# Kernel tuning notes

Hardware: AMD Instinct MI355X
Metric: run time of the kernel (lower is better)

Reference implementation:

```python
import jax, jax.numpy as jnp
import numpy as np

N = 50000      # nodes
E = 1600000    # edges
H = 128        # hidden_dim
P = 28         # pocket_dim
G = 256        # graphs in the batch
EPS = 1e-5     # BatchNorm eps


def setup_inputs() -> dict:
    key = jax.random.key(0)
    ks = jax.random.split(key, 24)
    s = 0.05
    inp = {
        "x": jax.random.normal(ks[0], (N, 7), jnp.float32),
        "edge_index": jax.random.randint(ks[1], (2, E), 0, N, jnp.int64),
        "batch": jnp.sort(jax.random.randint(ks[2], (N,), 0, G, jnp.int64)),
        "pocket_features": jax.random.normal(ks[3], (P,), jnp.float32),
        # GCN conv weights (first layer 7->128, layers 2..3 stacked 128->128)
        "conv0_W": jax.random.normal(ks[4], (7, H), jnp.float32) * s,
        "conv0_b": jnp.zeros((H,), jnp.float32),
        "convs_W": jax.random.normal(ks[5], (2, H, H), jnp.float32) * s,
        "convs_b": jnp.zeros((2, H), jnp.float32),
        # BatchNorm (eval mode) params per layer, stacked [3, H]
        "bn_gamma": jnp.ones((3, H), jnp.float32),
        "bn_beta": jnp.zeros((3, H), jnp.float32),
        "bn_mean": jax.random.normal(ks[6], (3, H), jnp.float32) * 0.1,
        "bn_var": jax.random.uniform(ks[7], (3, H), jnp.float32, 0.5, 1.5),
        # pocket MLP 28->64->64
        "pmlp_W1": jax.random.normal(ks[8], (P, 64), jnp.float32) * s,
        "pmlp_b1": jnp.zeros((64,), jnp.float32),
        "pmlp_W2": jax.random.normal(ks[9], (64, 64), jnp.float32) * s,
        "pmlp_b2": jnp.zeros((64,), jnp.float32),
        # Bilinear: torch weight shape [out=64, in1=H, in2=64]
        "bil_W": jax.random.normal(ks[10], (64, H, 64), jnp.float32) * s,
        "bil_b": jnp.zeros((64,), jnp.float32),
        # classifier 64->32->1
        "cls_W1": jax.random.normal(ks[11], (64, 32), jnp.float32) * s,
        "cls_b1": jnp.zeros((32,), jnp.float32),
        "cls_W2": jax.random.normal(ks[12], (32, 1), jnp.float32) * s,
        "cls_b2": jnp.zeros((1,), jnp.float32),
    }
    return inp


def _gcn(x, W, b, src, dst, dinv):
    """PyG GCNConv: sym-normalized aggregation with added self loops."""
    h = x @ W                                  # [N, H']
    norm = dinv[src] * dinv[dst]               # [E]
    agg = jax.ops.segment_sum(norm[:, None] * h[src], dst, num_segments=N)
    agg = agg + (dinv * dinv)[:, None] * h     # self-loop contribution
    return agg + b


def reference(x, edge_index, batch, pocket_features,
              conv0_W, conv0_b, convs_W, convs_b,
              bn_gamma, bn_beta, bn_mean, bn_var,
              pmlp_W1, pmlp_b1, pmlp_W2, pmlp_b2,
              bil_W, bil_b, cls_W1, cls_b1, cls_W2, cls_b2):
    src, dst = edge_index[0], edge_index[1]
    # degree over targets, with +1 for the self loop
    deg = jax.ops.segment_sum(jnp.ones((E,), x.dtype), dst, num_segments=N) + 1.0
    dinv = jax.lax.rsqrt(deg)

    h = x
    for i in range(3):
        W = conv0_W if i == 0 else convs_W[i - 1]
        b = conv0_b if i == 0 else convs_b[i - 1]
        h = _gcn(h, W, b, src, dst, dinv)
        # BatchNorm1d in eval mode; dropout = identity in eval
        h = bn_gamma[i] * (h - bn_mean[i]) * jax.lax.rsqrt(bn_var[i] + EPS) + bn_beta[i]
        h = jax.nn.relu(h)

    # global_mean_pool over graph ids
    sums = jax.ops.segment_sum(h, batch, num_segments=G)              # [G, H]
    cnt = jax.ops.segment_sum(jnp.ones((N,), h.dtype), batch, num_segments=G)
    ligand = sums / jnp.maximum(cnt, 1.0)[:, None]                    # [G, H]

    pk = jax.nn.relu(pocket_features @ pmlp_W1 + pmlp_b1) @ pmlp_W2 + pmlp_b2  # [64]
    pk = jnp.broadcast_to(pk, (G, 64))

    inter = jnp.einsum('bi,oij,bj->bo', ligand, bil_W, pk) + bil_b    # [G, 64]
    z = jax.nn.relu(inter @ cls_W1 + cls_b1) @ cls_W2 + cls_b2        # [G, 1]
    return z[:, 0]
```

## Files before the change

kernel.cpp:

```cpp
#include <hip/hip_runtime.h>

#define EPSBN 1e-5f
#define BCAP 12288
#define CSRL_CAP 13312
#define OVCAP 262144
#define INS_CAP 24
#define INS_STRIDE 25

#if defined(__has_builtin)
#if __has_builtin(__builtin_amdgcn_cvt_pk_f32_fp8) && __has_builtin(__builtin_amdgcn_cvt_pk_fp8_f32)
#define HAS_CVT_FP8 1
#endif
#endif

typedef float v2f_t __attribute__((ext_vector_type(2)));
typedef __attribute__((ext_vector_type(8))) short bf16x8;
typedef __attribute__((ext_vector_type(4))) float f32x4;

__device__ inline unsigned short f2bf(float f) {
    unsigned int u = __float_as_uint(f);
    u += 0x7fffu + ((u >> 16) & 1u);
    return (unsigned short)(u >> 16);
}

__device__ inline float fp8_dec_byte(int b) {
    int s = (b >> 7) & 1, e = (b >> 3) & 15, m = b & 7;
    float v = (e == 0) ? ldexpf((float)m, -9) : ldexpf((float)(8 + m), e - 10);
    return s ? -v : v;
}
__device__ inline unsigned int fp8_enc(float x) {
    unsigned int u = __float_as_uint(x);
    unsigned int s = u >> 31;
    u &= 0x7fffffffu;
    float a = __uint_as_float(u);
    unsigned int code;
    if (a >= 0.015625f) {
        if (a > 448.0f) code = 0x7E;
        else {
            int exp = (int)(u >> 23) - 127;
            unsigned int mant = u & 0x7fffffu;
            unsigned int keep = mant >> 20;
            unsigned int rest = mant & 0xfffffu;
            code = ((unsigned int)(exp + 7) << 3) | keep;
            unsigned int rnd = (rest > 0x80000u) || (rest == 0x80000u && (code & 1));
            code += rnd;
            if (code > 0x7E) code = 0x7E;
        }
    } else {
        code = (unsigned int)(a * 512.0f + 0.5f);
    }
    return (s << 7) | code;
}

__device__ __forceinline__ void fp8x8_dec(uint2 w, float* v) {
#ifdef HAS_CVT_FP8
    v2f_t l0 = __builtin_amdgcn_cvt_pk_f32_fp8((int)w.x, false);
    v2f_t h0 = __builtin_amdgcn_cvt_pk_f32_fp8((int)w.x, true);
    v2f_t l1 = __builtin_amdgcn_cvt_pk_f32_fp8((int)w.y, false);
    v2f_t h1 = __builtin_amdgcn_cvt_pk_f32_fp8((int)w.y, true);
    v[0] = l0[0]; v[1] = l0[1]; v[2] = h0[0]; v[3] = h0[1];
    v[4] = l1[0]; v[5] = l1[1]; v[6] = h1[0]; v[7] = h1[1];
#else
    v[0] = fp8_dec_byte(w.x & 255);        v[1] = fp8_dec_byte((w.x >> 8) & 255);
    v[2] = fp8_dec_byte((w.x >> 16) & 255); v[3] = fp8_dec_byte(w.x >> 24);
    v[4] = fp8_dec_byte(w.y & 255);        v[5] = fp8_dec_byte((w.y >> 8) & 255);
    v[6] = fp8_dec_byte((w.y >> 16) & 255); v[7] = fp8_dec_byte(w.y >> 24);
#endif
}

__global__ void setup_kernel(int* __restrict__ tails, int ntail,
                             const int* __restrict__ batch, int* __restrict__ gstart,
                             int n, int g,
                             const float* __restrict__ conv0_b, const float* __restrict__ convs_b,
                             const float* __restrict__ gamma, const float* __restrict__ beta,
                             const float* __restrict__ mean, const float* __restrict__ var,
                             float* __restrict__ sc, float* __restrict__ sh,
                             const float* __restrict__ convs_W, unsigned short* __restrict__ Wp,
                             const float* __restrict__ pf, const float* __restrict__ W1,
                             const float* __restrict__ b1, const float* __restrict__ W2,
                             const float* __restrict__ b2, const float* __restrict__ bilW,
                             float* __restrict__ M) {
    int t = threadIdx.x;
    int i = blockIdx.x * 256 + t;
    if (i < ntail * 32) tails[i] = 0;
    if (i < 384) {
        int l = i >> 7, f = i & 127;
        float bias = (l == 0) ? conv0_b[f] : convs_b[(l - 1) * 128 + f];
        float s = gamma[i] * rsqrtf(var[i] + EPSBN);
        sc[i] = s;
        sh[i] = fmaf(s, bias - mean[i], beta[i]);
    }
    if (i < 32768) {
        int l = i >> 14;
        int fidx = i & 16383;
        int j  = fidx & 7;
        int ln = (fidx >> 3) & 63;
        int nt = (fidx >> 9) & 7;
        int kk = fidx >> 12;
        int k = kk * 32 + (ln >> 4) * 8 + j;
        int c = nt * 16 + (ln & 15);
        Wp[i] = f2bf(convs_W[l * 16384 + k * 128 + c]);
    }
    if (i < n) {
        int b = batch[i];
        int bp = (i == 0) ? -1 : batch[i - 1];
        for (int q = bp + 1; q <= b; ++q) gstart[q] = i;
        if (i == n - 1) {
            for (int q = b + 1; q <= g; ++q) gstart[q] = n;
        }
    }
    if (blockIdx.x < 32) {
        __shared__ float h1s[64];
        __shared__ float spk[64];
        if (t < 64) {
            float acc = b1[t];
            #pragma unroll
            for (int k = 0; k < 28; ++k) acc = fmaf(pf[k], W1[k * 64 + t], acc);
            h1s[t] = fmaxf(acc, 0.f);
        }
        __syncthreads();
        if (t < 64) {
            float acc2 = b2[t];
            for (int k = 0; k < 64; ++k) acc2 = fmaf(h1s[k], W2[k * 64 + t], acc2);
            spk[t] = acc2;
        }
        __syncthreads();
        if (i < 64 * 128) {
            const float* wr = bilW + (size_t)i * 64;
            float acc = 0.f;
            #pragma unroll 8
            for (int j = 0; j < 64; ++j) acc = fmaf(wr[j], spk[j], acc);
            M[i] = acc;
        }
    }
}

__launch_bounds__(256)
__global__ void bucket_kernel(const int* __restrict__ src, const int* __restrict__ dst,
                              unsigned int* __restrict__ buckets, int* __restrict__ tails,
                              unsigned int* __restrict__ ovf, int e, int nwq) {
    __shared__ unsigned int buf[256 * INS_STRIDE];
    __shared__ int cnt[256];
    __shared__ int basee[256];
    int t = threadIdx.x;
    cnt[t] = 0;
    __syncthreads();
    int c0 = blockIdx.x * 2048;
    int c1 = min(c0 + 2048, e);
    for (int i = c0 + t; i < c1; i += 256) {
        int d = dst[i];
        int bb = d >> 8;
        unsigned int val = (unsigned int)src[i] | ((unsigned int)d << 16);
        int pos = atomicAdd(&cnt[bb], 1);
        if (pos < INS_CAP) buf[bb * INS_STRIDE + pos] = val;
        else {
            int op = atomicAdd(&tails[nwq * 32], 1);
            if (op < OVCAP) ovf[op] = val;
        }
    }
    __syncthreads();
    int lane = t & 63, wv = t >> 6;
    int bb0 = wv * 64;
    {
        int b = bb0 + lane;
        int c = (b < nwq) ? min(cnt[b], INS_CAP) : 0;
        basee[b] = c ? atomicAdd(&tails[b * 32], c) : 0;
    }
    for (int k = 0; k < 64; ++k) {
        int b = bb0 + k;
        if (b >= nwq) break;
        int c = min(cnt[b], INS_CAP);
        if (c == 0) continue;
        int g = basee[b];
        if (lane < c) {
            unsigned int v = buf[b * INS_STRIDE + lane];
            int gp = g + lane;
            if (gp < BCAP) buckets[(size_t)b * BCAP + gp] = v;
            else {
                int op = atomicAdd(&tails[nwq * 32], 1);
                if (op < OVCAP) ovf[op] = v;
            }
        }
    }
}

__launch_bounds__(256)
__global__ void build_csr(const unsigned int* __restrict__ buckets,
                          const int* __restrict__ tails, const unsigned int* __restrict__ ovf,
                          unsigned short* __restrict__ csr, int* __restrict__ deg,
                          int* __restrict__ offs, float* __restrict__ dinv,
                          int n, int nwq) {
    __shared__ unsigned short csrL[CSRL_CAP];
    __shared__ int degL[256], curL[256], offsL[256], cntW[256];
    __shared__ int wsum4[4];
    __shared__ int wstart;
    int b = blockIdx.x, t = threadIdx.x;
    int lo = b << 8;
    int hi = min(lo + 256, n);
    int nw = hi - lo;
    int ovn = min(tails[nwq * 32], OVCAP);
    cntW[t] = (t < nwq) ? min(tails[t * 32], BCAP) : 0;
    degL[t] = 0;
    __syncthreads();
    for (int i = t; i < ovn; i += 256)
        atomicAdd(&cntW[(ovf[i] >> 16) >> 8], 1);
    __syncthreads();
    if (t == 0) {
        int s = 0;
        for (int w = 0; w < b; ++w) s += cntW[w];
        wstart = s;
    }
    int myvalid = min(tails[b * 32], BCAP);
    const unsigned int* myb = buckets + (size_t)b * BCAP;
    for (int i = t; i < myvalid; i += 256)
        atomicAdd(&degL[(myb[i] >> 16) & 255], 1);
    for (int i = t; i < ovn; i += 256) {
        unsigned int v = ovf[i];
        int d = v >> 16;
        if (d >= lo && d < hi) atomicAdd(&degL[d & 255], 1);
    }
    __syncthreads();
    {
        int lane = t & 63, wv = t >> 6;
        int v = degL[t];
        int sc0 = v;
        #pragma unroll
        for (int o = 1; o < 64; o <<= 1) {
            int u = __shfl_up(sc0, o);
            if (lane >= o) sc0 += u;
        }
        if (lane == 63) wsum4[wv] = sc0;
        __syncthreads();
        int wb = 0;
        for (int q = 0; q < wv; ++q) wb += wsum4[q];
        offsL[t] = wb + sc0 - v;
        curL[t] = offsL[t];
    }
    __syncthreads();
    for (int i = t; i < myvalid; i += 256) {
        unsigned int v = myb[i];
        int pos = atomicAdd(&curL[(v >> 16) & 255], 1);
        if (pos < CSRL_CAP) csrL[pos] = (unsigned short)(v & 0xffffu);
    }
    for (int i = t; i < ovn; i += 256) {
        unsigned int v = ovf[i];
        int d = v >> 16;
        if (d >= lo && d < hi) {
            int pos = atomicAdd(&curL[d & 255], 1);
            if (pos < CSRL_CAP) csrL[pos] = (unsigned short)(v & 0xffffu);
        }
    }
    __syncthreads();
    int base = wstart;
    int total = min(cntW[b], CSRL_CAP);
    for (int i = t; i < total; i += 256)
        csr[base + i] = csrL[i];
    if (t < nw) {
        int dgi = degL[t];
        deg[lo + t] = dgi;
        offs[lo + t] = base + offsL[t];
        dinv[lo + t] = rsqrtf((float)dgi + 1.0f);
    }
}

__device__ __forceinline__ void dense_fp8_out(const unsigned short* hL,
                                              const unsigned short* __restrict__ Wp,
                                              unsigned char* __restrict__ out8,
                                              int b0n, int n, int lane, int wv) {
    f32x4 acc0 = {0.f, 0.f, 0.f, 0.f};
    f32x4 acc1 = {0.f, 0.f, 0.f, 0.f};
    int r = lane & 15, g = lane >> 4;
    int nt0 = wv * 2, nt1 = nt0 + 1;
    #pragma unroll
    for (int kk = 0; kk < 4; ++kk) {
        bf16x8 a  = *(const bf16x8*)(hL + r * 136 + kk * 32 + g * 8);
        bf16x8 b0 = *(const bf16x8*)(Wp + ((kk * 8 + nt0) * 64 + lane) * 8);
        bf16x8 b1 = *(const bf16x8*)(Wp + ((kk * 8 + nt1) * 64 + lane) * 8);
        acc0 = __builtin_amdgcn_mfma_f32_16x16x32_bf16(a, b0, acc0, 0, 0, 0);
        acc1 = __builtin_amdgcn_mfma_f32_16x16x32_bf16(a, b1, acc1, 0, 0, 0);
    }
    #pragma unroll
    for (int j = 0; j < 4; ++j) {
        int node = b0n + g * 4 + j;
        if (node < n) {
            unsigned char q0, q1;
#ifdef HAS_CVT_FP8
            q0 = (unsigned char)(__builtin_amdgcn_cvt_pk_fp8_f32(acc0[j], acc0[j], 0, false) & 0xff);
            q1 = (unsigned char)(__builtin_amdgcn_cvt_pk_fp8_f32(acc1[j], acc1[j], 0, false) & 0xff);
#else
            q0 = (unsigned char)fp8_enc(acc0[j]);
            q1 = (unsigned char)fp8_enc(acc1[j]);
#endif
            out8[(size_t)node * 128 + nt0 * 16 + r] = q0;
            out8[(size_t)node * 128 + nt1 * 16 + r] = q1;
        }
    }
}

__launch_bounds__(256)
__global__ void layer0f_kernel(const float* __restrict__ x, const unsigned short* __restrict__ csr,
                               const int* __restrict__ offs, const int* __restrict__ degi,
                               const float* __restrict__ dinv, const float* __restrict__ W,
                               const float* __restrict__ sc, const float* __restrict__ sh,
                               const unsigned short* __restrict__ Wp,
                               unsigned char* __restrict__ out8, int n) {
    __shared__ float sW[7 * 128];
    __shared__ float ssc[128], ssh[128];
    __shared__ unsigned short hL[16 * 136];
    int t = threadIdx.x;
    for (int i = t; i < 7 * 128; i += 256) sW[i] = W[i];
    if (t < 128) { ssc[t] = sc[t]; ssh[t] = sh[t]; }
    __syncthreads();
    int lane = t & 63, wv = t >> 6;
    int b0n = blockIdx.x * 16;
    int e = lane >> 3, f = lane & 7;
    for (int nd = 0; nd < 4; ++nd) {
        int node = b0n + wv * 4 + nd;
        if (node < n) {
            int off = offs[node], cnt = degi[node];
            float di = dinv[node];
            float acc = 0.f, accB = 0.f;
            for (int b0 = 0; b0 < cnt; b0 += 64) {
                int j = b0 + lane;
                int s = 0; float dv = 0.f;
                if (j < cnt) { s = csr[off + j]; dv = dinv[s]; }
                int m = cnt - b0; if (m > 64) m = 64;
                int m16 = (m + 15) & ~15;
                for (int i2 = 0; i2 < m16; i2 += 16) {
                    int ss1 = __shfl(s, i2 + e);
                    int ss2 = __shfl(s, i2 + 8 + e);
                    float d1 = __shfl(dv, i2 + e);
                    float d2 = __shfl(dv, i2 + 8 + e);
                    float v1 = 0.f, v2 = 0.f;
                    if (f < 7) {
                        v1 = d1 * x[(size_t)ss1 * 7 + f];
                        v2 = d2 * x[(size_t)ss2 * 7 + f];
                    }
                    acc += v1; accB += v2;
                }
            }
            acc += accB;
            acc += __shfl_xor(acc, 8);
            acc += __shfl_xor(acc, 16);
            acc += __shfl_xor(acc, 32);
            float self = (f < 7) ? x[(size_t)node * 7 + f] : 0.f;
            float xa = di * (acc + di * self);
            float xk[7];
            #pragma unroll
            for (int k = 0; k < 7; ++k) xk[k] = __shfl(xa, k);
            int fo = lane * 2;
            float o0 = 0.f, o1 = 0.f;
            #pragma unroll
            for (int k = 0; k < 7; ++k) {
                o0 = fmaf(xk[k], sW[k * 128 + fo], o0);
                o1 = fmaf(xk[k], sW[k * 128 + fo + 1], o1);
            }
            o0 = fmaxf(fmaf(ssc[fo],     o0, ssh[fo]),     0.f);
            o1 = fmaxf(fmaf(ssc[fo + 1], o1, ssh[fo + 1]), 0.f);
            unsigned int p = (unsigned int)f2bf(o0) | ((unsigned int)f2bf(o1) << 16);
            *(unsigned int*)(&hL[(wv * 4 + nd) * 136 + fo]) = p;
        }
    }
    __syncthreads();
    dense_fp8_out(hL, Wp, out8, b0n, n, lane, wv);
}

template<int DENSE>
__launch_bounds__(256)
__global__ void aggf_kernel(const unsigned int* __restrict__ hw, const unsigned short* __restrict__ csr,
                            const int* __restrict__ offs, const int* __restrict__ degi,
                            const float* __restrict__ dinv,
                            const float* __restrict__ sc, const float* __restrict__ shv,
                            const unsigned short* __restrict__ Wp,
                            unsigned char* __restrict__ out8,
                            float* __restrict__ outF, int n) {
    __shared__ unsigned short hL[16 * 136];
    int t = threadIdx.x, lane = t & 63, wv = t >> 6;
    int fl = lane & 15, grp = lane >> 4;
    int b0n = blockIdx.x * 16;
    for (int nd = 0; nd < 4; ++nd) {
        int node = b0n + wv * 4 + nd;
        if (node < n) {
            float di = dinv[node];
            int off = offs[node], cnt = degi[node];
            float a[8];
            #pragma unroll
            for (int i = 0; i < 8; ++i) a[i] = 0.f;
            for (int c0 = 0; c0 < cnt; c0 += 64) {
                int j = c0 + lane;
                int s = 0; float dv = 0.f;
                if (j < cnt) { s = csr[off + j]; dv = dinv[s]; }
                int m = cnt - c0; if (m > 64) m = 64;
                int m16 = (m + 15) & ~15;
                for (int e = 0; e < m16; e += 16) {
                    #pragma unroll
                    for (int u = 0; u < 4; ++u) {
                        int jj = e + u * 4 + grp;
                        int ss = __shfl(s, jj);
                        float nn = __shfl(dv, jj);
                        uint2 w = *(const uint2*)(hw + (size_t)ss * 32 + fl * 2);
                        float v[8];
                        fp8x8_dec(w, v);
                        #pragma unroll
                        for (int i = 0; i < 8; ++i) a[i] = fmaf(nn, v[i], a[i]);
                    }
                }
            }
            #pragma unroll
            for (int i = 0; i < 8; ++i) {
                a[i] += __shfl_xor(a[i], 16);
                a[i] += __shfl_xor(a[i], 32);
            }
            if (grp == 0) {
                uint2 ws = *(const uint2*)(hw + (size_t)node * 32 + fl * 2);
                float sv[8];
                fp8x8_dec(ws, sv);
                int f0 = fl * 8;
                float vo[8];
                #pragma unroll
                for (int i = 0; i < 8; ++i) {
                    float vv = (a[i] + di * sv[i]) * di;
                    vo[i] = fmaxf(fmaf(sc[f0 + i], vv, shv[f0 + i]), 0.f);
                }
                if (DENSE) {
                    uint4 P;
                    P.x = (unsigned int)f2bf(vo[0]) | ((unsigned int)f2bf(vo[1]) << 16);
                    P.y = (unsigned int)f2bf(vo[2]) | ((unsigned int)f2bf(vo[3]) << 16);
                    P.z = (unsigned int)f2bf(vo[4]) | ((unsigned int)f2bf(vo[5]) << 16);
                    P.w = (unsigned int)f2bf(vo[6]) | ((unsigned int)f2bf(vo[7]) << 16);
                    *(uint4*)(&hL[(wv * 4 + nd) * 136 + f0]) = P;
                } else {
                    float4 o0 = make_float4(vo[0], vo[1], vo[2], vo[3]);
                    float4 o1 = make_float4(vo[4], vo[5], vo[6], vo[7]);
                    *(float4*)(outF + (size_t)node * 128 + f0)     = o0;
                    *(float4*)(outF + (size_t)node * 128 + f0 + 4) = o1;
                }
            }
        }
    }
    if (DENSE) {
        __syncthreads();
        dense_fp8_out(hL, Wp, out8, b0n, n, lane, wv);
    }
}

__launch_bounds__(128)
__global__ void final_kernel(const float* __restrict__ h, const int* __restrict__ gstart,
                             const float* __restrict__ M, const float* __restrict__ bil_b,
                             const float* __restrict__ cW1, const float* __restrict__ cb1,
                             const float* __restrict__ cW2, const float* __restrict__ cb2,
                             float* __restrict__ out) {
    __shared__ float lig[128];
    __shared__ float inter[64];
    __shared__ float hc[32];
    int g = blockIdx.x, t = threadIdx.x;
    int s = gstart[g], e = gstart[g + 1];
    float a0 = 0.f, a1 = 0.f, a2 = 0.f, a3 = 0.f;
    int i = s;
    for (; i + 4 <= e; i += 4) {
        a0 += h[(size_t)(i + 0) * 128 + t];
        a1 += h[(size_t)(i + 1) * 128 + t];
        a2 += h[(size_t)(i + 2) * 128 + t];
        a3 += h[(size_t)(i + 3) * 128 + t];
    }
    for (; i < e; ++i) a0 += h[(size_t)i * 128 + t];
    float c = (float)(e - s); if (c < 1.f) c = 1.f;
    lig[t] = ((a0 + a1) + (a2 + a3)) / c;
    __syncthreads();
    if (t < 64) {
        float acc = bil_b[t];
        const float* mr = M + (size_t)t * 128;
        #pragma unroll 8
        for (int k = 0; k < 128; ++k) acc = fmaf(lig[k], mr[k], acc);
        inter[t] = acc;
    }
    __syncthreads();
    if (t < 32) {
        float acc = cb1[t];
        #pragma unroll 8
        for (int o = 0; o < 64; ++o) acc = fmaf(inter[o], cW1[o * 32 + t], acc);
        hc[t] = fmaxf(acc, 0.f);
    }
    __syncthreads();
    if (t == 0) {
        float acc = cb2[0];
        #pragma unroll
        for (int j = 0; j < 32; ++j) acc = fmaf(hc[j], cW2[j], acc);
        out[g] = acc;
    }
}

extern "C" void kernel_launch(void* const* d_in, const int* in_sizes, int n_in,
                              void* d_out, int out_size, void* d_ws, size_t ws_size,
                              hipStream_t stream) {
    const float* x        = (const float*)d_in[0];
    const int*   edge     = (const int*)d_in[1];
    const int*   batch    = (const int*)d_in[2];
    const float* pocket   = (const float*)d_in[3];
    const float* conv0_W  = (const float*)d_in[4];
    const float* conv0_b  = (const float*)d_in[5];
    const float* convs_W  = (const float*)d_in[6];
    const float* convs_b  = (const float*)d_in[7];
    const float* bn_gamma = (const float*)d_in[8];
    const float* bn_beta  = (const float*)d_in[9];
    const float* bn_mean  = (const float*)d_in[10];
    const float* bn_var   = (const float*)d_in[11];
    const float* pmlp_W1  = (const float*)d_in[12];
    const float* pmlp_b1  = (const float*)d_in[13];
    const float* pmlp_W2  = (const float*)d_in[14];
    const float* pmlp_b2  = (const float*)d_in[15];
    const float* bil_W    = (const float*)d_in[16];
    const float* bil_b    = (const float*)d_in[17];
    const float* cls_W1   = (const float*)d_in[18];
    const float* cls_b1   = (const float*)d_in[19];
    const float* cls_W2   = (const float*)d_in[20];
    const float* cls_b2   = (const float*)d_in[21];

    const int N = in_sizes[0] / 7;
    const int E = in_sizes[1] / 2;
    const int G = out_size;
    const int* srcA = edge;
    const int* dstA = edge + E;
    const int NB  = (N + 255) / 256;
    const int NWQ = (N + 255) >> 8;
    const int NBL = (N + 15) / 16;

    char* p = (char*)d_ws;
    auto alloc = [&](size_t bytes) -> void* {
        void* r = (void*)p;
        p += (bytes + 255) & ~(size_t)255;
        return r;
    };
    int*   tails    = (int*)alloc((size_t)(NWQ + 1) * 32 * 4);
    unsigned int* buckets = (unsigned int*)alloc((size_t)NWQ * BCAP * 4);
    unsigned int* ovf     = (unsigned int*)alloc((size_t)OVCAP * 4);
    int*   deg      = (int*)alloc((size_t)N * 4);
    int*   offs     = (int*)alloc((size_t)N * 4);
    float* dinv     = (float*)alloc((size_t)N * 4);
    unsigned short* csr = (unsigned short*)alloc((size_t)E * 2);
    unsigned char* bufH8a = (unsigned char*)alloc((size_t)N * 128);
    unsigned char* bufH8b = (unsigned char*)alloc((size_t)N * 128);
    float* bufF     = (float*)alloc((size_t)N * 128 * 4);
    int*   gstart   = (int*)alloc((size_t)(G + 1) * 4);
    float* M        = (float*)alloc(64 * 128 * 4);
    float* sc       = (float*)alloc(384 * 4);
    float* shv      = (float*)alloc(384 * 4);
    unsigned short* Wp = (unsigned short*)alloc((size_t)2 * 16384 * 2);

    setup_kernel<<<NB, 256, 0, stream>>>(tails, NWQ + 1, batch, gstart, N, G,
                                         conv0_b, convs_b, bn_gamma, bn_beta, bn_mean, bn_var,
                                         sc, shv, convs_W, Wp,
                                         pocket, pmlp_W1, pmlp_b1, pmlp_W2, pmlp_b2, bil_W, M);
    bucket_kernel<<<(E + 2047) / 2048, 256, 0, stream>>>(srcA, dstA, buckets, tails, ovf,
                                                         E, NWQ);
    build_csr<<<NWQ, 256, 0, stream>>>(buckets, tails, ovf, csr, deg, offs, dinv, N, NWQ);

    layer0f_kernel<<<NBL, 256, 0, stream>>>(x, csr, offs, deg, dinv, conv0_W,
                                            sc, shv, Wp, bufH8a, N);
    aggf_kernel<1><<<NBL, 256, 0, stream>>>((const unsigned int*)bufH8a, csr, offs, deg, dinv,
                                            sc + 128, shv + 128, Wp + 16384, bufH8b, nullptr, N);
    aggf_kernel<0><<<NBL, 256, 0, stream>>>((const unsigned int*)bufH8b, csr, offs, deg, dinv,
                                            sc + 256, shv + 256, nullptr, nullptr, bufF, N);

    final_kernel<<<G, 128, 0, stream>>>(bufF, gstart, M, bil_b, cls_W1, cls_b1, cls_W2, cls_b2,
                                        (float*)d_out);
}
```

Baseline: 284.2 us.

## Pack source dinv into padded CSR entries and compute degrees during bucketing

Degrees are now counted with global atomics in the bucketing pass, and a separate kernel computes dinv and per-window padded sizes. The CSR becomes 32-bit entries that pack the source id with a bf16 copy of its dinv, and each node's list is padded to a multiple of 16 with zero entries. This removes the dependent dinv[src] gather and the shuffle broadcasts from the aggregation loops and lets each lane load edges directly with unrolled independent gathers. In exchange it adds global atomics, an extra launch, larger CSR traffic, and bf16 rounding of the normalisation; the final pooling loop is also unrolled to 8 accumulators.

```diff
diff --git a/kernel.cpp b/kernel.cpp
--- a/kernel.cpp
+++ b/kernel.cpp
@@ -2,7 +2,6 @@
 
 #define EPSBN 1e-5f
 #define BCAP 12288
-#define CSRL_CAP 13312
 #define OVCAP 262144
 #define INS_CAP 24
 #define INS_STRIDE 25
@@ -70,6 +69,7 @@
 
 __global__ void setup_kernel(int* __restrict__ tails, int ntail,
                              const int* __restrict__ batch, int* __restrict__ gstart,
+                             int* __restrict__ deg,
                              int n, int g,
                              const float* __restrict__ conv0_b, const float* __restrict__ convs_b,
                              const float* __restrict__ gamma, const float* __restrict__ beta,
@@ -102,6 +102,7 @@
         Wp[i] = f2bf(convs_W[l * 16384 + k * 128 + c]);
     }
     if (i < n) {
+        deg[i] = 0;
         int b = batch[i];
         int bp = (i == 0) ? -1 : batch[i - 1];
         for (int q = bp + 1; q <= b; ++q) gstart[q] = i;
@@ -138,7 +139,8 @@
 __launch_bounds__(256)
 __global__ void bucket_kernel(const int* __restrict__ src, const int* __restrict__ dst,
                               unsigned int* __restrict__ buckets, int* __restrict__ tails,
-                              unsigned int* __restrict__ ovf, int e, int nwq) {
+                              unsigned int* __restrict__ ovf, int* __restrict__ deg,
+                              int e, int nwq) {
     __shared__ unsigned int buf[256 * INS_STRIDE];
     __shared__ int cnt[256];
     __shared__ int basee[256];
@@ -150,6 +152,7 @@
     for (int i = c0 + t; i < c1; i += 256) {
         int d = dst[i];
         int bb = d >> 8;
+        atomicAdd(&deg[d], 1);
         unsigned int val = (unsigned int)src[i] | ((unsigned int)d << 16);
         int pos = atomicAdd(&cnt[bb], 1);
         if (pos < INS_CAP) buf[bb * INS_STRIDE + pos] = val;
@@ -185,82 +188,86 @@
 }
 
 __launch_bounds__(256)
-__global__ void build_csr(const unsigned int* __restrict__ buckets,
-                          const int* __restrict__ tails, const unsigned int* __restrict__ ovf,
-                          unsigned short* __restrict__ csr, int* __restrict__ deg,
-                          int* __restrict__ offs, float* __restrict__ dinv,
-                          int n, int nwq) {
-    __shared__ unsigned short csrL[CSRL_CAP];
-    __shared__ int degL[256], curL[256], offsL[256], cntW[256];
+__global__ void dinv_kernel(const int* __restrict__ deg, float* __restrict__ dinv,
+                            int* __restrict__ winPad, int n) {
+    __shared__ int ws[4];
+    int b = blockIdx.x, t = threadIdx.x;
+    int i = b * 256 + t;
+    int d = (i < n) ? deg[i] : 0;
+    if (i < n) dinv[i] = rsqrtf((float)d + 1.0f);
+    int pad = (i < n) ? ((d + 15) & ~15) : 0;
+    int lane = t & 63, wv = t >> 6;
+    int s = pad;
+    #pragma unroll
+    for (int o = 1; o < 64; o <<= 1) s += __shfl_xor(s, o);
+    if (lane == 0) ws[wv] = s;
+    __syncthreads();
+    if (t == 0) winPad[b] = ws[0] + ws[1] + ws[2] + ws[3];
+}
+
+__launch_bounds__(256)
+__global__ void build_csr2(const unsigned int* __restrict__ buckets,
+                           const int* __restrict__ tails, const unsigned int* __restrict__ ovf,
+                           const int* __restrict__ deg, const float* __restrict__ dinv,
+                           const int* __restrict__ winPad,
+                           unsigned int* __restrict__ csr2, int* __restrict__ offs,
+                           int n, int nwq) {
+    __shared__ int curL[256];
     __shared__ int wsum4[4];
     __shared__ int wstart;
     int b = blockIdx.x, t = threadIdx.x;
     int lo = b << 8;
     int hi = min(lo + 256, n);
     int nw = hi - lo;
-    int ovn = min(tails[nwq * 32], OVCAP);
-    cntW[t] = (t < nwq) ? min(tails[t * 32], BCAP) : 0;
-    degL[t] = 0;
-    __syncthreads();
-    for (int i = t; i < ovn; i += 256)
-        atomicAdd(&cntW[(ovf[i] >> 16) >> 8], 1);
-    __syncthreads();
     if (t == 0) {
         int s = 0;
-        for (int w = 0; w < b; ++w) s += cntW[w];
+        for (int w = 0; w < b; ++w) s += winPad[w];
         wstart = s;
     }
+    int dpad = (t < nw) ? ((deg[lo + t] + 15) & ~15) : 0;
+    int lane = t & 63, wv = t >> 6;
+    int sc0 = dpad;
+    #pragma unroll
+    for (int o = 1; o < 64; o <<= 1) {
+        int u = __shfl_up(sc0, o);
+        if (lane >= o) sc0 += u;
+    }
+    if (lane == 63) wsum4[wv] = sc0;
+    __syncthreads();
+    int wb = 0;
+    for (int q = 0; q < wv; ++q) wb += wsum4[q];
+    int myoff = wb + sc0 - dpad;
+    curL[t] = myoff;
+    int total = wsum4[0] + wsum4[1] + wsum4[2] + wsum4[3];
+    int base = wstart;
+    for (int i = t; i < total; i += 256) csr2[base + i] = 0u;
+    __syncthreads();
     int myvalid = min(tails[b * 32], BCAP);
     const unsigned int* myb = buckets + (size_t)b * BCAP;
-    for (int i = t; i < myvalid; i += 256)
-        atomicAdd(&degL[(myb[i] >> 16) & 255], 1);
-    for (int i = t; i < ovn; i += 256) {
-        unsigned int v = ovf[i];
-        int d = v >> 16;
-        if (d >= lo && d < hi) atomicAdd(&degL[d & 255], 1);
-    }
-    __syncthreads();
-    {
-        int lane = t & 63, wv = t >> 6;
-        int v = degL[t];
-        int sc0 = v;
-        #pragma unroll
-        for (int o = 1; o < 64; o <<= 1) {
-            int u = __shfl_up(sc0, o);
-            if (lane >= o) sc0 += u;
-        }
-        if (lane == 63) wsum4[wv] = sc0;
-        __syncthreads();
-        int wb = 0;
-        for (int q = 0; q < wv; ++q) wb += wsum4[q];
-        offsL[t] = wb + sc0 - v;
-        curL[t] = offsL[t];
-    }
-    __syncthreads();
     for (int i = t; i < myvalid; i += 256) {
         unsigned int v = myb[i];
-        int pos = atomicAdd(&curL[(v >> 16) & 255], 1);
-        if (pos < CSRL_CAP) csrL[pos] = (unsigned short)(v & 0xffffu);
-    }
+        int dl = (v >> 16) & 255;
+        int s = v & 0xffff;
+        int pos = atomicAdd(&curL[dl], 1);
+        if (pos < total) {
+            unsigned int enc = (unsigned int)f2bf(dinv[s]);
+            csr2[base + pos] = (unsigned int)s | (enc << 16);
+        }
+    }
+    int ovn = min(tails[nwq * 32], OVCAP);
     for (int i = t; i < ovn; i += 256) {
         unsigned int v = ovf[i];
         int d = v >> 16;
         if (d >= lo && d < hi) {
+            int s = v & 0xffff;
             int pos = atomicAdd(&curL[d & 255], 1);
-            if (pos < CSRL_CAP) csrL[pos] = (unsigned short)(v & 0xffffu);
-        }
-    }
-    __syncthreads();
-    int base = wstart;
-    int total = min(cntW[b], CSRL_CAP);
-    for (int i = t; i < total; i += 256)
-        csr[base + i] = csrL[i];
-    if (t < nw) {
-        int dgi = degL[t];
-        deg[lo + t] = dgi;
-        offs[lo + t] = base + offsL[t];
-        dinv[lo + t] = rsqrtf((float)dgi + 1.0f);
-    }
+            if (pos < total) {
+                unsigned int enc = (unsigned int)f2bf(dinv[s]);
+                csr2[base + pos] = (unsigned int)s | (enc << 16);
+            }
+        }
+    }
+    if (t < nw) offs[lo + t] = base + myoff;
 }
 
 __device__ __forceinline__ void dense_fp8_out(const unsigned short* hL,
@@ -298,7 +305,7 @@
 }
 
 __launch_bounds__(256)
-__global__ void layer0f_kernel(const float* __restrict__ x, const unsigned short* __restrict__ csr,
+__global__ void layer0f_kernel(const float* __restrict__ x, const unsigned int* __restrict__ csr2,
                                const int* __restrict__ offs, const int* __restrict__ degi,
                                const float* __restrict__ dinv, const float* __restrict__ W,
                                const float* __restrict__ sc, const float* __restrict__ sh,
@@ -316,34 +323,30 @@
     int e = lane >> 3, f = lane & 7;
     for (int nd = 0; nd < 4; ++nd) {
         int node = b0n + wv * 4 + nd;
-        if (node < n) {
-            int off = offs[node], cnt = degi[node];
-            float di = dinv[node];
-            float acc = 0.f, accB = 0.f;
-            for (int b0 = 0; b0 < cnt; b0 += 64) {
-                int j = b0 + lane;
-                int s = 0; float dv = 0.f;
-                if (j < cnt) { s = csr[off + j]; dv = dinv[s]; }
-                int m = cnt - b0; if (m > 64) m = 64;
-                int m16 = (m + 15) & ~15;
-                for (int i2 = 0; i2 < m16; i2 += 16) {
-                    int ss1 = __shfl(s, i2 + e);
-                    int ss2 = __shfl(s, i2 + 8 + e);
-                    float d1 = __shfl(dv, i2 + e);
-                    float d2 = __shfl(dv, i2 + 8 + e);
-                    float v1 = 0.f, v2 = 0.f;
-                    if (f < 7) {
-                        v1 = d1 * x[(size_t)ss1 * 7 + f];
-                        v2 = d2 * x[(size_t)ss2 * 7 + f];
-                    }
-                    acc += v1; accB += v2;
-                }
-            }
-            acc += accB;
+        bool ok = node < n;
+        int off  = ok ? offs[node] : 0;
+        int cntp = ok ? ((degi[node] + 15) & ~15) : 0;
+        float di = ok ? dinv[node] : 0.f;
+        float self = (ok && f < 7) ? x[(size_t)node * 7 + f] : 0.f;
+        float acc = 0.f;
+        for (int c0 = 0; c0 < cntp; c0 += 16) {
+            unsigned int e4[2];
+            #pragma unroll
+            for (int u = 0; u < 2; ++u) e4[u] = csr2[off + c0 + u * 8 + e];
+            float vA[2];
+            #pragma unroll
+            for (int u = 0; u < 2; ++u) {
+                int ss = e4[u] & 0xffff;
+                vA[u] = (f < 7) ? x[(size_t)ss * 7 + f] : 0.f;
+            }
+            #pragma unroll
+            for (int u = 0; u < 2; ++u)
+                acc = fmaf(__uint_as_float(e4[u] & 0xffff0000u), vA[u], acc);
+        }
+        if (ok) {
             acc += __shfl_xor(acc, 8);
             acc += __shfl_xor(acc, 16);
             acc += __shfl_xor(acc, 32);
-            float self = (f < 7) ? x[(size_t)node * 7 + f] : 0.f;
             float xa = di * (acc + di * self);
             float xk[7];
             #pragma unroll
@@ -367,7 +370,7 @@
 
 template<int DENSE>
 __launch_bounds__(256)
-__global__ void aggf_kernel(const unsigned int* __restrict__ hw, const unsigned short* __restrict__ csr,
+__global__ void aggf_kernel(const unsigned int* __restrict__ hw, const unsigned int* __restrict__ csr2,
                             const int* __restrict__ offs, const int* __restrict__ degi,
                             const float* __restrict__ dinv,
                             const float* __restrict__ sc, const float* __restrict__ shv,
@@ -380,61 +383,60 @@
     int b0n = blockIdx.x * 16;
     for (int nd = 0; nd < 4; ++nd) {
         int node = b0n + wv * 4 + nd;
-        if (node < n) {
-            float di = dinv[node];
-            int off = offs[node], cnt = degi[node];
-            float a[8];
-            #pragma unroll
-            for (int i = 0; i < 8; ++i) a[i] = 0.f;
-            for (int c0 = 0; c0 < cnt; c0 += 64) {
-                int j = c0 + lane;
-                int s = 0; float dv = 0.f;
-                if (j < cnt) { s = csr[off + j]; dv = dinv[s]; }
-                int m = cnt - c0; if (m > 64) m = 64;
-                int m16 = (m + 15) & ~15;
-                for (int e = 0; e < m16; e += 16) {
-                    #pragma unroll
-                    for (int u = 0; u < 4; ++u) {
-                        int jj = e + u * 4 + grp;
-                        int ss = __shfl(s, jj);
-                        float nn = __shfl(dv, jj);
-                        uint2 w = *(const uint2*)(hw + (size_t)ss * 32 + fl * 2);
-                        float v[8];
-                        fp8x8_dec(w, v);
-                        #pragma unroll
-                        for (int i = 0; i < 8; ++i) a[i] = fmaf(nn, v[i], a[i]);
-                    }
-                }
-            }
+        bool ok = node < n;
+        int off  = ok ? offs[node] : 0;
+        int cntp = ok ? ((degi[node] + 15) & ~15) : 0;
+        float di = ok ? dinv[node] : 0.f;
+        uint2 ws = ok ? *(const uint2*)(hw + (size_t)node * 32 + fl * 2) : make_uint2(0u, 0u);
+        float a[8];
+        #pragma unroll
+        for (int i = 0; i < 8; ++i) a[i] = 0.f;
+        for (int c0 = 0; c0 < cntp; c0 += 16) {
+            unsigned int e4[4];
+            #pragma unroll
+            for (int u = 0; u < 4; ++u) e4[u] = csr2[off + c0 + u * 4 + grp];
+            uint2 w[4];
+            #pragma unroll
+            for (int u = 0; u < 4; ++u) {
+                int ss = e4[u] & 0xffff;
+                w[u] = *(const uint2*)(hw + (size_t)ss * 32 + fl * 2);
+            }
+            #pragma unroll
+            for (int u = 0; u < 4; ++u) {
+                float nn = __uint_as_float(e4[u] & 0xffff0000u);
+                float v[8];
+                fp8x8_dec(w[u], v);
+                #pragma unroll
+                for (int i = 0; i < 8; ++i) a[i] = fmaf(nn, v[i], a[i]);
+            }
+        }
+        #pragma unroll
+        for (int i = 0; i < 8; ++i) {
+            a[i] += __shfl_xor(a[i], 16);
+            a[i] += __shfl_xor(a[i], 32);
+        }
+        if (grp == 0 && ok) {
+            float sv[8];
+            fp8x8_dec(ws, sv);
+            int f0 = fl * 8;
+            float vo[8];
             #pragma unroll
             for (int i = 0; i < 8; ++i) {
-                a[i] += __shfl_xor(a[i], 16);
-                a[i] += __shfl_xor(a[i], 32);
-            }
-            if (grp == 0) {
-                uint2 ws = *(const uint2*)(hw + (size_t)node * 32 + fl * 2);
-                float sv[8];
-                fp8x8_dec(ws, sv);
-                int f0 = fl * 8;
-                float vo[8];
-                #pragma unroll
-                for (int i = 0; i < 8; ++i) {
-                    float vv = (a[i] + di * sv[i]) * di;
-                    vo[i] = fmaxf(fmaf(sc[f0 + i], vv, shv[f0 + i]), 0.f);
-                }
-                if (DENSE) {
-                    uint4 P;
-                    P.x = (unsigned int)f2bf(vo[0]) | ((unsigned int)f2bf(vo[1]) << 16);
-                    P.y = (unsigned int)f2bf(vo[2]) | ((unsigned int)f2bf(vo[3]) << 16);
-                    P.z = (unsigned int)f2bf(vo[4]) | ((unsigned int)f2bf(vo[5]) << 16);
-                    P.w = (unsigned int)f2bf(vo[6]) | ((unsigned int)f2bf(vo[7]) << 16);
-                    *(uint4*)(&hL[(wv * 4 + nd) * 136 + f0]) = P;
-                } else {
-                    float4 o0 = make_float4(vo[0], vo[1], vo[2], vo[3]);
-                    float4 o1 = make_float4(vo[4], vo[5], vo[6], vo[7]);
-                    *(float4*)(outF + (size_t)node * 128 + f0)     = o0;
-                    *(float4*)(outF + (size_t)node * 128 + f0 + 4) = o1;
-                }
+                float vv = (a[i] + di * sv[i]) * di;
+                vo[i] = fmaxf(fmaf(sc[f0 + i], vv, shv[f0 + i]), 0.f);
+            }
+            if (DENSE) {
+                uint4 P;
+                P.x = (unsigned int)f2bf(vo[0]) | ((unsigned int)f2bf(vo[1]) << 16);
+                P.y = (unsigned int)f2bf(vo[2]) | ((unsigned int)f2bf(vo[3]) << 16);
+                P.z = (unsigned int)f2bf(vo[4]) | ((unsigned int)f2bf(vo[5]) << 16);
+                P.w = (unsigned int)f2bf(vo[6]) | ((unsigned int)f2bf(vo[7]) << 16);
+                *(uint4*)(&hL[(wv * 4 + nd) * 136 + f0]) = P;
+            } else {
+                float4 o0 = make_float4(vo[0], vo[1], vo[2], vo[3]);
+                float4 o1 = make_float4(vo[4], vo[5], vo[6], vo[7]);
+                *(float4*)(outF + (size_t)node * 128 + f0)     = o0;
+                *(float4*)(outF + (size_t)node * 128 + f0 + 4) = o1;
             }
         }
     }
@@ -455,17 +457,18 @@
     __shared__ float hc[32];
     int g = blockIdx.x, t = threadIdx.x;
     int s = gstart[g], e = gstart[g + 1];
-    float a0 = 0.f, a1 = 0.f, a2 = 0.f, a3 = 0.f;
+    float a[8];
+    #pragma unroll
+    for (int q = 0; q < 8; ++q) a[q] = 0.f;
     int i = s;
-    for (; i + 4 <= e; i += 4) {
-        a0 += h[(size_t)(i + 0) * 128 + t];
-        a1 += h[(size_t)(i + 1) * 128 + t];
-        a2 += h[(size_t)(i + 2) * 128 + t];
-        a3 += h[(size_t)(i + 3) * 128 + t];
-    }
-    for (; i < e; ++i) a0 += h[(size_t)i * 128 + t];
+    for (; i + 8 <= e; i += 8) {
+        #pragma unroll
+        for (int q = 0; q < 8; ++q)
+            a[q] += h[(size_t)(i + q) * 128 + t];
+    }
+    for (; i < e; ++i) a[0] += h[(size_t)i * 128 + t];
     float c = (float)(e - s); if (c < 1.f) c = 1.f;
-    lig[t] = ((a0 + a1) + (a2 + a3)) / c;
+    lig[t] = (((a[0] + a[1]) + (a[2] + a[3])) + ((a[4] + a[5]) + (a[6] + a[7]))) / c;
     __syncthreads();
     if (t < 64) {
         float acc = bil_b[t];
@@ -537,7 +540,8 @@
     int*   deg      = (int*)alloc((size_t)N * 4);
     int*   offs     = (int*)alloc((size_t)N * 4);
     float* dinv     = (float*)alloc((size_t)N * 4);
-    unsigned short* csr = (unsigned short*)alloc((size_t)E * 2);
+    int*   winPad   = (int*)alloc((size_t)NWQ * 4);
+    unsigned int* csr2 = (unsigned int*)alloc(((size_t)E + 15 * (size_t)N + 4096) * 4);
     unsigned char* bufH8a = (unsigned char*)alloc((size_t)N * 128);
     unsigned char* bufH8b = (unsigned char*)alloc((size_t)N * 128);
     float* bufF     = (float*)alloc((size_t)N * 128 * 4);
@@ -547,19 +551,21 @@
     float* shv      = (float*)alloc(384 * 4);
     unsigned short* Wp = (unsigned short*)alloc((size_t)2 * 16384 * 2);
 
-    setup_kernel<<<NB, 256, 0, stream>>>(tails, NWQ + 1, batch, gstart, N, G,
+    setup_kernel<<<NB, 256, 0, stream>>>(tails, NWQ + 1, batch, gstart, deg, N, G,
                                          conv0_b, convs_b, bn_gamma, bn_beta, bn_mean, bn_var,
                                          sc, shv, convs_W, Wp,
                                          pocket, pmlp_W1, pmlp_b1, pmlp_W2, pmlp_b2, bil_W, M);
-    bucket_kernel<<<(E + 2047) / 2048, 256, 0, stream>>>(srcA, dstA, buckets, tails, ovf,
+    bucket_kernel<<<(E + 2047) / 2048, 256, 0, stream>>>(srcA, dstA, buckets, tails, ovf, deg,
                                                          E, NWQ);
-    build_csr<<<NWQ, 256, 0, stream>>>(buckets, tails, ovf, csr, deg, offs, dinv, N, NWQ);
-
-    layer0f_kernel<<<NBL, 256, 0, stream>>>(x, csr, offs, deg, dinv, conv0_W,
+    dinv_kernel<<<NWQ, 256, 0, stream>>>(deg, dinv, winPad, N);
+    build_csr2<<<NWQ, 256, 0, stream>>>(buckets, tails, ovf, deg, dinv, winPad,
+                                        csr2, offs, N, NWQ);
+
+    layer0f_kernel<<<NBL, 256, 0, stream>>>(x, csr2, offs, deg, dinv, conv0_W,
                                             sc, shv, Wp, bufH8a, N);
-    aggf_kernel<1><<<NBL, 256, 0, stream>>>((const unsigned int*)bufH8a, csr, offs, deg, dinv,
+    aggf_kernel<1><<<NBL, 256, 0, stream>>>((const unsigned int*)bufH8a, csr2, offs, deg, dinv,
                                             sc + 128, shv + 128, Wp + 16384, bufH8b, nullptr, N);
-    aggf_kernel<0><<<NBL, 256, 0, stream>>>((const unsigned int*)bufH8b, csr, offs, deg, dinv,
+    aggf_kernel<0><<<NBL, 256, 0, stream>>>((const unsigned int*)bufH8b, csr2, offs, deg, dinv,
                                             sc + 256, shv + 256, nullptr, nullptr, bufF, N);
 
     final_kernel<<<G, 128, 0, stream>>>(bufF, gstart, M, bil_b, cls_W1, cls_b1, cls_W2, cls_b2,
```

Measured after the change: 359.0 us. 1.26x slower.
